# Kernel tuning notes

Hardware: AMD Instinct MI355X
Metric: run time of the kernel (lower is better)

The kernel has to match this reference:

```python
import jax, jax.numpy as jnp
import numpy as np

N_NODES = 40000
N_EDGES = 640000
D = 128
NEG_SLOPE = 0.2
EPS = 0.0  # init_eps=0, learn_eps=False -> constant buffer


def setup_inputs() -> dict:
    key = jax.random.key(0)
    ks = jax.random.split(key, 9)
    return {
        "feat": jax.random.normal(ks[0], (N_NODES, D), dtype=jnp.float32),
        "W_src": jax.random.normal(ks[1], (D, D), dtype=jnp.float32) * 0.1,
        "W_dst": jax.random.normal(ks[2], (D, D), dtype=jnp.float32) * 0.1,
        "W_src2": jax.random.normal(ks[3], (D, D), dtype=jnp.float32) * 0.1,
        "W_dst2": jax.random.normal(ks[4], (D, D), dtype=jnp.float32) * 0.1,
        "attn_l": jax.random.normal(ks[5], (D,), dtype=jnp.float32) * 0.1,
        "attn_r": jax.random.normal(ks[6], (D,), dtype=jnp.float32) * 0.1,
        "src": jax.random.randint(ks[7], (N_EDGES,), 0, N_NODES, dtype=jnp.int32),
        "dst": jax.random.randint(ks[8], (N_EDGES,), 0, N_NODES, dtype=jnp.int32),
    }


def reference(feat, W_src, W_dst, W_src2, W_dst2, attn_l, attn_r, src, dst):
    n = feat.shape[0]
    # Four linear projections (no bias), nn.Linear applies x @ W.T
    fs1 = feat @ W_src.T    # [N, D] -> messages for GIN sum
    fd1 = feat @ W_dst.T    # [N, D] -> self term
    fs2 = feat @ W_src2.T   # [N, D] -> attention-weighted messages
    fd2 = feat @ W_dst2.T   # [N, D]

    # GAT-style per-node attention logits
    el = jnp.sum(fs2 * attn_l, axis=-1)  # [N]
    er = jnp.sum(fd2 * attn_r, axis=-1)  # [N]

    # Per-edge score: u_add_v + leaky_relu
    e = el[src] + er[dst]                                   # [E]
    e = jnp.where(e >= 0, e, NEG_SLOPE * e)

    # edge_softmax: segment-wise softmax over edges grouped by dst
    seg_max = jax.ops.segment_max(e, dst, num_segments=n)   # [N]
    seg_max = jnp.where(jnp.isfinite(seg_max), seg_max, 0.0)
    ex = jnp.exp(e - seg_max[dst])                          # [E]
    denom = jax.ops.segment_sum(ex, dst, num_segments=n)    # [N]
    a = ex / denom[dst]                                     # [E]

    # update_all(copy_u, sum): plain neighbor sum of fs1
    neigh = jax.ops.segment_sum(fs1[src], dst, num_segments=n)            # [N, D]
    # update_all(u_mul_e, sum): attention-weighted sum of fs2
    add_ft = jax.ops.segment_sum(fs2[src] * a[:, None], dst, num_segments=n)  # [N, D]

    rst = (1.0 + EPS) * fd1 + neigh + add_ft
    return rst
```

## Files before the change

### kernel.cpp

```cpp
#include <hip/hip_runtime.h>
#include <math.h>

#define N_NODES 40000
#define N_EDGES 640000
#define D 128
#define NEG_SLOPE 0.2f
#define BCAP 64

typedef __bf16 bf16x8 __attribute__((ext_vector_type(8)));
typedef float f32x4 __attribute__((ext_vector_type(4)));

__device__ __forceinline__ unsigned short f2bf(float f) {
    unsigned int u = __float_as_uint(f);
    return (unsigned short)((u + 0x7fffu + ((u >> 16) & 1u)) >> 16);
}
__device__ __forceinline__ float bflo(unsigned int u) { return __uint_as_float(u << 16); }
__device__ __forceinline__ float bfhi(unsigned int u) { return __uint_as_float(u & 0xffff0000u); }

__global__ void k_zero_v(uint4* __restrict__ cnt4,
                         const float* __restrict__ Ws2, const float* __restrict__ Wd2,
                         const float* __restrict__ attn_l, const float* __restrict__ attn_r,
                         float* __restrict__ v_l, float* __restrict__ v_r) {
    if (blockIdx.x == 40) {
        int t = threadIdx.x;
        if (t < 128) {
            float s = 0.0f;
            for (int j = 0; j < D; ++j) s += attn_l[j] * Ws2[j * D + t];
            v_l[t] = s;
        } else {
            int k = t - 128;
            float s = 0.0f;
            for (int j = 0; j < D; ++j) s += attn_r[j] * Wd2[j * D + k];
            v_r[k] = s;
        }
        return;
    }
    int i = blockIdx.x * 256 + threadIdx.x;
    if (i < 10000) cnt4[i] = make_uint4(0, 0, 0, 0);
}

__global__ void k_setup(const float* __restrict__ Ws, const float* __restrict__ Ws2,
                        const float* __restrict__ Wd,
                        unsigned short* __restrict__ Wfrag,
                        const float* __restrict__ v_l, const float* __restrict__ v_r,
                        const int* __restrict__ src, const int* __restrict__ dst,
                        int* __restrict__ cnt, unsigned short* __restrict__ bucket,
                        const float* __restrict__ feat, unsigned int* __restrict__ featb,
                        float* __restrict__ el, float* __restrict__ er) {
    if (blockIdx.x >= 2692) {
        int idx = blockIdx.x - 2692;
        int row = idx * 16 + (threadIdx.x >> 4);
        int c   = threadIdx.x & 15;
        const float* fp = feat + (size_t)row * D + c * 8;
        float4 p = *(const float4*)fp;
        float4 q = *(const float4*)(fp + 4);
        uint4 u;
        u.x = (unsigned int)f2bf(p.x) | ((unsigned int)f2bf(p.y) << 16);
        u.y = (unsigned int)f2bf(p.z) | ((unsigned int)f2bf(p.w) << 16);
        u.z = (unsigned int)f2bf(q.x) | ((unsigned int)f2bf(q.y) << 16);
        u.w = (unsigned int)f2bf(q.z) | ((unsigned int)f2bf(q.w) << 16);
        *(uint4*)(featb + (size_t)row * 64 + c * 4) = u;
        const float* vlp = v_l + c * 8;
        const float* vrp = v_r + c * 8;
        float4 l0 = *(const float4*)vlp, l1 = *(const float4*)(vlp + 4);
        float4 r0 = *(const float4*)vrp, r1 = *(const float4*)(vrp + 4);
        float sl = p.x*l0.x + p.y*l0.y + p.z*l0.z + p.w*l0.w
                 + q.x*l1.x + q.y*l1.y + q.z*l1.z + q.w*l1.w;
        float sr = p.x*r0.x + p.y*r0.y + p.z*r0.z + p.w*r0.w
                 + q.x*r1.x + q.y*r1.y + q.z*r1.z + q.w*r1.w;
        #pragma unroll
        for (int w = 1; w <= 8; w <<= 1) {
            sl += __shfl_xor(sl, w);
            sr += __shfl_xor(sr, w);
        }
        if (c == 0) { el[row] = sl; er[row] = sr; }
        return;
    }
    if (blockIdx.x >= 192) {
        int e = (blockIdx.x - 192) * 256 + threadIdx.x;
        if (e < N_EDGES) {
            int d = dst[e];
            int slot = atomicAdd(&cnt[d], 1);
            if (slot < BCAP) bucket[(size_t)d * BCAP + slot] = (unsigned short)src[e];
        }
        return;
    }
    int idx = blockIdx.x * 256 + threadIdx.x;
    int e    = idx & 7;
    int lane = (idx >> 3) & 63;
    int ks   = (idx >> 9) & 3;
    int ct   = (idx >> 11) & 7;
    int m    = idx >> 14;
    int col  = ct * 16 + (lane & 15);
    int k    = ks * 32 + (lane >> 4) * 8 + e;
    const float* W = (m == 0) ? Ws : (m == 1) ? Ws2 : Wd;
    Wfrag[idx] = f2bf(W[col * D + k]);
}

__global__ __launch_bounds__(256) void k_aggregate(
    const int* __restrict__ cnt, const unsigned short* __restrict__ bucket,
    const float* __restrict__ el, const float* __restrict__ er,
    const unsigned int* __restrict__ featb,
    unsigned int* __restrict__ agg1b, unsigned int* __restrict__ agg2b)
{
    const int node = blockIdx.x * 4 + (threadIdx.x >> 6);
    const int lane = threadIdx.x & 63;
    if (node >= N_NODES) return;
    int deg = cnt[node];
    deg = (deg > BCAP) ? BCAP : deg;

    const int q = lane & 15;
    const int g = lane >> 4;
    float A1[8], A2[8];
    #pragma unroll
    for (int c = 0; c < 8; ++c) { A1[c] = 0.f; A2[c] = 0.f; }

    if (deg > 0) {
        const int base = node * BCAP;
        const float ern = er[node];
        int s_l = 0;
        float e = -INFINITY;
        if (lane < deg) {
            s_l = bucket[base + lane];
            e = el[s_l] + ern;
            e = (e >= 0.f) ? e : NEG_SLOPE * e;
        }
        float mx = e;
        #pragma unroll
        for (int w = 32; w >= 1; w >>= 1) mx = fmaxf(mx, __shfl_xor(mx, w));
        float p = (lane < deg) ? __expf(e - mx) : 0.f;
        float ssum = p;
        #pragma unroll
        for (int w = 32; w >= 1; w >>= 1) ssum += __shfl_xor(ssum, w);
        float a_l = p / ssum;

        const int dup = (deg + 15) & ~15;
        for (int i = 0; i < dup; i += 16) {
            uint4 v[4];
            float av[4], wf[4];
            #pragma unroll
            for (int j = 0; j < 4; ++j) {
                int eidx = i + j * 4 + g;
                int s = __shfl(s_l, eidx);
                av[j] = __shfl(a_l, eidx);
                wf[j] = (eidx < deg) ? 1.0f : 0.0f;
                v[j] = *(const uint4*)(featb + (size_t)s * 64 + q * 4);
            }
            #pragma unroll
            for (int j = 0; j < 4; ++j) {
                float x0 = bflo(v[j].x), x1 = bfhi(v[j].x);
                float x2 = bflo(v[j].y), x3 = bfhi(v[j].y);
                float x4 = bflo(v[j].z), x5 = bfhi(v[j].z);
                float x6 = bflo(v[j].w), x7 = bfhi(v[j].w);
                A1[0] += wf[j] * x0; A2[0] += av[j] * x0;
                A1[1] += wf[j] * x1; A2[1] += av[j] * x1;
                A1[2] += wf[j] * x2; A2[2] += av[j] * x2;
                A1[3] += wf[j] * x3; A2[3] += av[j] * x3;
                A1[4] += wf[j] * x4; A2[4] += av[j] * x4;
                A1[5] += wf[j] * x5; A2[5] += av[j] * x5;
                A1[6] += wf[j] * x6; A2[6] += av[j] * x6;
                A1[7] += wf[j] * x7; A2[7] += av[j] * x7;
            }
        }
        #pragma unroll
        for (int c = 0; c < 8; ++c) {
            A1[c] += __shfl_xor(A1[c], 16); A1[c] += __shfl_xor(A1[c], 32);
            A2[c] += __shfl_xor(A2[c], 16); A2[c] += __shfl_xor(A2[c], 32);
        }
    }

    if (lane < 16) {
        uint4 u1, u2;
        u1.x = (unsigned int)f2bf(A1[0]) | ((unsigned int)f2bf(A1[1]) << 16);
        u1.y = (unsigned int)f2bf(A1[2]) | ((unsigned int)f2bf(A1[3]) << 16);
        u1.z = (unsigned int)f2bf(A1[4]) | ((unsigned int)f2bf(A1[5]) << 16);
        u1.w = (unsigned int)f2bf(A1[6]) | ((unsigned int)f2bf(A1[7]) << 16);
        u2.x = (unsigned int)f2bf(A2[0]) | ((unsigned int)f2bf(A2[1]) << 16);
        u2.y = (unsigned int)f2bf(A2[2]) | ((unsigned int)f2bf(A2[3]) << 16);
        u2.z = (unsigned int)f2bf(A2[4]) | ((unsigned int)f2bf(A2[5]) << 16);
        u2.w = (unsigned int)f2bf(A2[6]) | ((unsigned int)f2bf(A2[7]) << 16);
        *(uint4*)(agg1b + (size_t)node * 64 + q * 4) = u1;
        *(uint4*)(agg2b + (size_t)node * 64 + q * 4) = u2;
    }
}

__global__ __launch_bounds__(256) void k_gemm_all(
    const unsigned int* __restrict__ featb,
    const unsigned int* __restrict__ agg1b, const unsigned int* __restrict__ agg2b,
    const unsigned short* __restrict__ Wfrag, float* __restrict__ out)
{
    const int lane = threadIdx.x & 63;
    const int wave = threadIdx.x >> 6;
    const int tile = blockIdx.x >> 1;
    const int cth  = (blockIdx.x & 1) * 4;
    const int row0 = tile * 64 + wave * 16;
    const int arow = row0 + (lane & 15);
    const int koff = (lane >> 4) * 4;

    bf16x8 af[4], a1[4], a2[4];
    #pragma unroll
    for (int ks = 0; ks < 4; ++ks) {
        size_t o = (size_t)arow * 64 + ks * 16 + koff;
        af[ks] = *(const bf16x8*)(featb + o);
        a1[ks] = *(const bf16x8*)(agg1b + o);
        a2[ks] = *(const bf16x8*)(agg2b + o);
    }

    const bf16x8* wf0 = (const bf16x8*)Wfrag;
    const bf16x8* wf1 = wf0 + (size_t)(8 * 4) * 64;
    const bf16x8* wf2 = wf0 + (size_t)(2 * 8 * 4) * 64;

    f32x4 acc[4];
    #pragma unroll
    for (int c = 0; c < 4; ++c) acc[c] = (f32x4){0.f, 0.f, 0.f, 0.f};
    #pragma unroll
    for (int ks = 0; ks < 4; ++ks) {
        #pragma unroll
        for (int c = 0; c < 4; ++c) {
            const size_t bo = (size_t)((cth + c) * 4 + ks) * 64 + lane;
            acc[c] = __builtin_amdgcn_mfma_f32_16x16x32_bf16(af[ks], wf2[bo], acc[c], 0, 0, 0);
            acc[c] = __builtin_amdgcn_mfma_f32_16x16x32_bf16(a1[ks], wf0[bo], acc[c], 0, 0, 0);
            acc[c] = __builtin_amdgcn_mfma_f32_16x16x32_bf16(a2[ks], wf1[bo], acc[c], 0, 0, 0);
        }
    }

    const int rbase = row0 + (lane >> 4) * 4;
    const int cbase = lane & 15;
    #pragma unroll
    for (int c = 0; c < 4; ++c)
        #pragma unroll
        for (int r = 0; r < 4; ++r)
            out[(size_t)(rbase + r) * D + (cth + c) * 16 + cbase] = acc[c][r];
}

extern "C" void kernel_launch(void* const* d_in, const int* in_sizes, int n_in,
                              void* d_out, int out_size, void* d_ws, size_t ws_size,
                              hipStream_t stream) {
    const float* feat   = (const float*)d_in[0];
    const float* W_src  = (const float*)d_in[1];
    const float* W_dst  = (const float*)d_in[2];
    const float* W_src2 = (const float*)d_in[3];
    const float* W_dst2 = (const float*)d_in[4];
    const float* attn_l = (const float*)d_in[5];
    const float* attn_r = (const float*)d_in[6];
    const int*   src    = (const int*)d_in[7];
    const int*   dst    = (const int*)d_in[8];
    float* out = (float*)d_out;

    char* w = (char*)d_ws;
    float* v_l = (float*)w;                       w += 128 * 4;
    float* v_r = (float*)w;                       w += 128 * 4;
    float* el  = (float*)w;                       w += N_NODES * 4;
    float* er  = (float*)w;                       w += N_NODES * 4;
    int* cnt   = (int*)w;                         w += N_NODES * 4;
    unsigned int* featb = (unsigned int*)w;       w += (size_t)N_NODES * 64 * 4;
    unsigned int* agg1b = (unsigned int*)w;       w += (size_t)N_NODES * 64 * 4;
    unsigned int* agg2b = (unsigned int*)w;       w += (size_t)N_NODES * 64 * 4;
    unsigned short* bucket = (unsigned short*)w;  w += (size_t)N_NODES * BCAP * 2;
    unsigned short* Wfrag = (unsigned short*)w;   w += 3 * 8 * 4 * 64 * 8 * 2;

    k_zero_v<<<41, 256, 0, stream>>>((uint4*)cnt, W_src2, W_dst2, attn_l, attn_r, v_l, v_r);

    k_setup<<<5192, 256, 0, stream>>>(W_src, W_src2, W_dst, Wfrag, v_l, v_r,
                                      src, dst, cnt, bucket, feat, featb, el, er);

    k_aggregate<<<(N_NODES + 3) / 4, 256, 0, stream>>>(cnt, bucket, el, er,
                                                       featb, agg1b, agg2b);

    k_gemm_all<<<1250, 256, 0, stream>>>(featb, agg1b, agg2b, Wfrag, out);
}
```

Before: 96.21 us.

## Prefetch first 32 neighbor rows before softmax and batch edge bucketing per thread

In the aggregate kernel, the first 32 neighbor feature rows are gathered before the softmax reduction runs, so gather latency overlaps the attention computation. The loop is split into an unconditional first 16, a conditional second 16, and a remainder loop. The setup kernel now processes four edges per thread in the bucketing blocks and reorders block roles so bucketing launches first, which reduces the grid size. This adds register pressure from eight uint4 prefetches and issues loads for padded lanes that all point at node 0.

```diff
diff --git a/kernel.cpp b/kernel.cpp
--- a/kernel.cpp
+++ b/kernel.cpp
@@ -47,54 +47,57 @@
                         int* __restrict__ cnt, unsigned short* __restrict__ bucket,
                         const float* __restrict__ feat, unsigned int* __restrict__ featb,
                         float* __restrict__ el, float* __restrict__ er) {
-    if (blockIdx.x >= 2692) {
-        int idx = blockIdx.x - 2692;
-        int row = idx * 16 + (threadIdx.x >> 4);
-        int c   = threadIdx.x & 15;
-        const float* fp = feat + (size_t)row * D + c * 8;
-        float4 p = *(const float4*)fp;
-        float4 q = *(const float4*)(fp + 4);
-        uint4 u;
-        u.x = (unsigned int)f2bf(p.x) | ((unsigned int)f2bf(p.y) << 16);
-        u.y = (unsigned int)f2bf(p.z) | ((unsigned int)f2bf(p.w) << 16);
-        u.z = (unsigned int)f2bf(q.x) | ((unsigned int)f2bf(q.y) << 16);
-        u.w = (unsigned int)f2bf(q.z) | ((unsigned int)f2bf(q.w) << 16);
-        *(uint4*)(featb + (size_t)row * 64 + c * 4) = u;
-        const float* vlp = v_l + c * 8;
-        const float* vrp = v_r + c * 8;
-        float4 l0 = *(const float4*)vlp, l1 = *(const float4*)(vlp + 4);
-        float4 r0 = *(const float4*)vrp, r1 = *(const float4*)(vrp + 4);
-        float sl = p.x*l0.x + p.y*l0.y + p.z*l0.z + p.w*l0.w
-                 + q.x*l1.x + q.y*l1.y + q.z*l1.z + q.w*l1.w;
-        float sr = p.x*r0.x + p.y*r0.y + p.z*r0.z + p.w*r0.w
-                 + q.x*r1.x + q.y*r1.y + q.z*r1.z + q.w*r1.w;
-        #pragma unroll
-        for (int w = 1; w <= 8; w <<= 1) {
-            sl += __shfl_xor(sl, w);
-            sr += __shfl_xor(sr, w);
-        }
-        if (c == 0) { el[row] = sl; er[row] = sr; }
+    if (blockIdx.x < 625) {
+        int t = blockIdx.x * 256 + threadIdx.x;
+        #pragma unroll
+        for (int j = 0; j < 4; ++j) {
+            int e = t + j * 160000;
+            int d = dst[e];
+            int s = src[e];
+            int slot = atomicAdd(&cnt[d], 1);
+            if (slot < BCAP) bucket[(size_t)d * BCAP + slot] = (unsigned short)s;
+        }
         return;
     }
-    if (blockIdx.x >= 192) {
-        int e = (blockIdx.x - 192) * 256 + threadIdx.x;
-        if (e < N_EDGES) {
-            int d = dst[e];
-            int slot = atomicAdd(&cnt[d], 1);
-            if (slot < BCAP) bucket[(size_t)d * BCAP + slot] = (unsigned short)src[e];
-        }
+    if (blockIdx.x < 817) {
+        int idx = (blockIdx.x - 625) * 256 + threadIdx.x;
+        int e    = idx & 7;
+        int lane = (idx >> 3) & 63;
+        int ks   = (idx >> 9) & 3;
+        int ct   = (idx >> 11) & 7;
+        int m    = idx >> 14;
+        int col  = ct * 16 + (lane & 15);
+        int k    = ks * 32 + (lane >> 4) * 8 + e;
+        const float* W = (m == 0) ? Ws : (m == 1) ? Ws2 : Wd;
+        Wfrag[idx] = f2bf(W[col * D + k]);
         return;
     }
-    int idx = blockIdx.x * 256 + threadIdx.x;
-    int e    = idx & 7;
-    int lane = (idx >> 3) & 63;
-    int ks   = (idx >> 9) & 3;
-    int ct   = (idx >> 11) & 7;
-    int m    = idx >> 14;
-    int col  = ct * 16 + (lane & 15);
-    int k    = ks * 32 + (lane >> 4) * 8 + e;
-    const float* W = (m == 0) ? Ws : (m == 1) ? Ws2 : Wd;
-    Wfrag[idx] = f2bf(W[col * D + k]);
+    int idx = blockIdx.x - 817;
+    int row = idx * 16 + (threadIdx.x >> 4);
+    int c   = threadIdx.x & 15;
+    const float* fp = feat + (size_t)row * D + c * 8;
+    float4 p = *(const float4*)fp;
+    float4 q = *(const float4*)(fp + 4);
+    uint4 u;
+    u.x = (unsigned int)f2bf(p.x) | ((unsigned int)f2bf(p.y) << 16);
+    u.y = (unsigned int)f2bf(p.z) | ((unsigned int)f2bf(p.w) << 16);
+    u.z = (unsigned int)f2bf(q.x) | ((unsigned int)f2bf(q.y) << 16);
+    u.w = (unsigned int)f2bf(q.z) | ((unsigned int)f2bf(q.w) << 16);
+    *(uint4*)(featb + (size_t)row * 64 + c * 4) = u;
+    const float* vlp = v_l + c * 8;
+    const float* vrp = v_r + c * 8;
+    float4 l0 = *(const float4*)vlp, l1 = *(const float4*)(vlp + 4);
+    float4 r0 = *(const float4*)vrp, r1 = *(const float4*)(vrp + 4);
+    float sl = p.x*l0.x + p.y*l0.y + p.z*l0.z + p.w*l0.w
+             + q.x*l1.x + q.y*l1.y + q.z*l1.z + q.w*l1.w;
+    float sr = p.x*r0.x + p.y*r0.y + p.z*r0.z + p.w*r0.w
+             + q.x*r1.x + q.y*r1.y + q.z*r1.z + q.w*r1.w;
+    #pragma unroll
+    for (int w = 1; w <= 8; w <<= 1) {
+        sl += __shfl_xor(sl, w);
+        sr += __shfl_xor(sr, w);
+    }
+    if (c == 0) { el[row] = sl; er[row] = sr; }
 }
 
 __global__ __launch_bounds__(256) void k_aggregate(
@@ -117,11 +120,20 @@
 
     if (deg > 0) {
         const int base = node * BCAP;
+        int s_l = bucket[base + lane];
+        if (lane >= deg) s_l = 0;
+
+        uint4 v[8];
+        #pragma unroll
+        for (int j = 0; j < 8; ++j) {
+            int eidx = (j >> 2) * 16 + (j & 3) * 4 + g;
+            int s = __shfl(s_l, eidx);
+            v[j] = *(const uint4*)(featb + (size_t)s * 64 + q * 4);
+        }
+
         const float ern = er[node];
-        int s_l = 0;
         float e = -INFINITY;
         if (lane < deg) {
-            s_l = bucket[base + lane];
             e = el[s_l] + ern;
             e = (e >= 0.f) ? e : NEG_SLOPE * e;
         }
@@ -134,34 +146,72 @@
         for (int w = 32; w >= 1; w >>= 1) ssum += __shfl_xor(ssum, w);
         float a_l = p / ssum;
 
-        const int dup = (deg + 15) & ~15;
-        for (int i = 0; i < dup; i += 16) {
-            uint4 v[4];
-            float av[4], wf[4];
+        #pragma unroll
+        for (int j = 0; j < 4; ++j) {
+            int eidx = (j & 3) * 4 + g;
+            float av = __shfl(a_l, eidx);
+            float wf = (eidx < deg) ? 1.0f : 0.0f;
+            float x0 = bflo(v[j].x), x1 = bfhi(v[j].x);
+            float x2 = bflo(v[j].y), x3 = bfhi(v[j].y);
+            float x4 = bflo(v[j].z), x5 = bfhi(v[j].z);
+            float x6 = bflo(v[j].w), x7 = bfhi(v[j].w);
+            A1[0] += wf * x0; A2[0] += av * x0;
+            A1[1] += wf * x1; A2[1] += av * x1;
+            A1[2] += wf * x2; A2[2] += av * x2;
+            A1[3] += wf * x3; A2[3] += av * x3;
+            A1[4] += wf * x4; A2[4] += av * x4;
+            A1[5] += wf * x5; A2[5] += av * x5;
+            A1[6] += wf * x6; A2[6] += av * x6;
+            A1[7] += wf * x7; A2[7] += av * x7;
+        }
+        if (deg > 16) {
             #pragma unroll
-            for (int j = 0; j < 4; ++j) {
-                int eidx = i + j * 4 + g;
-                int s = __shfl(s_l, eidx);
-                av[j] = __shfl(a_l, eidx);
-                wf[j] = (eidx < deg) ? 1.0f : 0.0f;
-                v[j] = *(const uint4*)(featb + (size_t)s * 64 + q * 4);
-            }
-            #pragma unroll
-            for (int j = 0; j < 4; ++j) {
+            for (int j = 4; j < 8; ++j) {
+                int eidx = 16 + (j & 3) * 4 + g;
+                float av = __shfl(a_l, eidx);
+                float wf = (eidx < deg) ? 1.0f : 0.0f;
                 float x0 = bflo(v[j].x), x1 = bfhi(v[j].x);
                 float x2 = bflo(v[j].y), x3 = bfhi(v[j].y);
                 float x4 = bflo(v[j].z), x5 = bfhi(v[j].z);
                 float x6 = bflo(v[j].w), x7 = bfhi(v[j].w);
-                A1[0] += wf[j] * x0; A2[0] += av[j] * x0;
-                A1[1] += wf[j] * x1; A2[1] += av[j] * x1;
-                A1[2] += wf[j] * x2; A2[2] += av[j] * x2;
-                A1[3] += wf[j] * x3; A2[3] += av[j] * x3;
-                A1[4] += wf[j] * x4; A2[4] += av[j] * x4;
-                A1[5] += wf[j] * x5; A2[5] += av[j] * x5;
-                A1[6] += wf[j] * x6; A2[6] += av[j] * x6;
-                A1[7] += wf[j] * x7; A2[7] += av[j] * x7;
+                A1[0] += wf * x0; A2[0] += av * x0;
+                A1[1] += wf * x1; A2[1] += av * x1;
+                A1[2] += wf * x2; A2[2] += av * x2;
+                A1[3] += wf * x3; A2[3] += av * x3;
+                A1[4] += wf * x4; A2[4] += av * x4;
+                A1[5] += wf * x5; A2[5] += av * x5;
+                A1[6] += wf * x6; A2[6] += av * x6;
+                A1[7] += wf * x7; A2[7] += av * x7;
             }
-        }
+            for (int i = 32; i < deg; i += 16) {
+                uint4 vt[4];
+                float av[4], wf[4];
+                #pragma unroll
+                for (int j = 0; j < 4; ++j) {
+                    int eidx = i + j * 4 + g;
+                    int s = __shfl(s_l, eidx);
+                    av[j] = __shfl(a_l, eidx);
+                    wf[j] = (eidx < deg) ? 1.0f : 0.0f;
+                    vt[j] = *(const uint4*)(featb + (size_t)s * 64 + q * 4);
+                }
+                #pragma unroll
+                for (int j = 0; j < 4; ++j) {
+                    float x0 = bflo(vt[j].x), x1 = bfhi(vt[j].x);
+                    float x2 = bflo(vt[j].y), x3 = bfhi(vt[j].y);
+                    float x4 = bflo(vt[j].z), x5 = bfhi(vt[j].z);
+                    float x6 = bflo(vt[j].w), x7 = bfhi(vt[j].w);
+                    A1[0] += wf[j] * x0; A2[0] += av[j] * x0;
+                    A1[1] += wf[j] * x1; A2[1] += av[j] * x1;
+                    A1[2] += wf[j] * x2; A2[2] += av[j] * x2;
+                    A1[3] += wf[j] * x3; A2[3] += av[j] * x3;
+                    A1[4] += wf[j] * x4; A2[4] += av[j] * x4;
+                    A1[5] += wf[j] * x5; A2[5] += av[j] * x5;
+                    A1[6] += wf[j] * x6; A2[6] += av[j] * x6;
+                    A1[7] += wf[j] * x7; A2[7] += av[j] * x7;
+                }
+            }
+        }
+
         #pragma unroll
         for (int c = 0; c < 8; ++c) {
             A1[c] += __shfl_xor(A1[c], 16); A1[c] += __shfl_xor(A1[c], 32);
@@ -261,7 +311,7 @@
 
     k_zero_v<<<41, 256, 0, stream>>>((uint4*)cnt, W_src2, W_dst2, attn_l, attn_r, v_l, v_r);
 
-    k_setup<<<5192, 256, 0, stream>>>(W_src, W_src2, W_dst, Wfrag, v_l, v_r,
+    k_setup<<<3317, 256, 0, stream>>>(W_src, W_src2, W_dst, Wfrag, v_l, v_r,
                                       src, dst, cnt, bucket, feat, featb, el, er);
 
     k_aggregate<<<(N_NODES + 3) / 4, 256, 0, stream>>>(cnt, bucket, el, er,
```

Result: slower. 98.73 us (+2.6%).

## Fuse neighbor aggregation and output GEMM into one kernel via LDS

Applied to the files above, without the earlier changes.

Merges the aggregation kernel and the MFMA GEMM kernel so each 1024-thread block aggregates 16 nodes into shared memory, then 8 waves compute the 16x128 output tile directly. This removes the global round-trip of the two bf16 aggregate buffers and one kernel launch. In exchange, half the waves sit idle during the GEMM phase, a block barrier is added, and each block reloads the weight fragments, with smaller GEMM tiles than before.

```diff
diff --git a/kernel.cpp b/kernel.cpp
--- a/kernel.cpp
+++ b/kernel.cpp
@@ -97,15 +97,19 @@
     Wfrag[idx] = f2bf(W[col * D + k]);
 }
 
-__global__ __launch_bounds__(256) void k_aggregate(
+__global__ __launch_bounds__(1024, 8) void k_agg_gemm(
     const int* __restrict__ cnt, const unsigned short* __restrict__ bucket,
     const float* __restrict__ el, const float* __restrict__ er,
-    const unsigned int* __restrict__ featb,
-    unsigned int* __restrict__ agg1b, unsigned int* __restrict__ agg2b)
+    const unsigned int* __restrict__ featb, const unsigned short* __restrict__ Wfrag,
+    float* __restrict__ out)
 {
-    const int node = blockIdx.x * 4 + (threadIdx.x >> 6);
+    __shared__ uint4 lds1[16][17];
+    __shared__ uint4 lds2[16][17];
+
+    const int wv   = threadIdx.x >> 6;
     const int lane = threadIdx.x & 63;
-    if (node >= N_NODES) return;
+    const int node = blockIdx.x * 16 + wv;
+
     int deg = cnt[node];
     deg = (deg > BCAP) ? BCAP : deg;
 
@@ -179,58 +183,38 @@
         u2.y = (unsigned int)f2bf(A2[2]) | ((unsigned int)f2bf(A2[3]) << 16);
         u2.z = (unsigned int)f2bf(A2[4]) | ((unsigned int)f2bf(A2[5]) << 16);
         u2.w = (unsigned int)f2bf(A2[6]) | ((unsigned int)f2bf(A2[7]) << 16);
-        *(uint4*)(agg1b + (size_t)node * 64 + q * 4) = u1;
-        *(uint4*)(agg2b + (size_t)node * 64 + q * 4) = u2;
-    }
-}
-
-__global__ __launch_bounds__(256) void k_gemm_all(
-    const unsigned int* __restrict__ featb,
-    const unsigned int* __restrict__ agg1b, const unsigned int* __restrict__ agg2b,
-    const unsigned short* __restrict__ Wfrag, float* __restrict__ out)
-{
-    const int lane = threadIdx.x & 63;
-    const int wave = threadIdx.x >> 6;
-    const int tile = blockIdx.x >> 1;
-    const int cth  = (blockIdx.x & 1) * 4;
-    const int row0 = tile * 64 + wave * 16;
-    const int arow = row0 + (lane & 15);
-    const int koff = (lane >> 4) * 4;
-
-    bf16x8 af[4], a1[4], a2[4];
-    #pragma unroll
-    for (int ks = 0; ks < 4; ++ks) {
-        size_t o = (size_t)arow * 64 + ks * 16 + koff;
-        af[ks] = *(const bf16x8*)(featb + o);
-        a1[ks] = *(const bf16x8*)(agg1b + o);
-        a2[ks] = *(const bf16x8*)(agg2b + o);
-    }
-
-    const bf16x8* wf0 = (const bf16x8*)Wfrag;
-    const bf16x8* wf1 = wf0 + (size_t)(8 * 4) * 64;
-    const bf16x8* wf2 = wf0 + (size_t)(2 * 8 * 4) * 64;
-
-    f32x4 acc[4];
-    #pragma unroll
-    for (int c = 0; c < 4; ++c) acc[c] = (f32x4){0.f, 0.f, 0.f, 0.f};
-    #pragma unroll
-    for (int ks = 0; ks < 4; ++ks) {
-        #pragma unroll
-        for (int c = 0; c < 4; ++c) {
-            const size_t bo = (size_t)((cth + c) * 4 + ks) * 64 + lane;
-            acc[c] = __builtin_amdgcn_mfma_f32_16x16x32_bf16(af[ks], wf2[bo], acc[c], 0, 0, 0);
-            acc[c] = __builtin_amdgcn_mfma_f32_16x16x32_bf16(a1[ks], wf0[bo], acc[c], 0, 0, 0);
-            acc[c] = __builtin_amdgcn_mfma_f32_16x16x32_bf16(a2[ks], wf1[bo], acc[c], 0, 0, 0);
-        }
-    }
-
-    const int rbase = row0 + (lane >> 4) * 4;
-    const int cbase = lane & 15;
-    #pragma unroll
-    for (int c = 0; c < 4; ++c)
-        #pragma unroll
-        for (int r = 0; r < 4; ++r)
-            out[(size_t)(rbase + r) * D + (cth + c) * 16 + cbase] = acc[c][r];
+        lds1[wv][q] = u1;
+        lds2[wv][q] = u2;
+    }
+    __syncthreads();
+
+    if (wv < 8) {
+        const int ct = wv;
+        const int r = lane & 15;
+        const int h = lane >> 4;
+        const int row0 = blockIdx.x * 16;
+
+        const bf16x8* wf0 = (const bf16x8*)Wfrag;
+        const bf16x8* wf1 = wf0 + (size_t)(8 * 4) * 64;
+        const bf16x8* wf2 = wf0 + (size_t)(2 * 8 * 4) * 64;
+
+        f32x4 acc = (f32x4){0.f, 0.f, 0.f, 0.f};
+        #pragma unroll
+        for (int ks = 0; ks < 4; ++ks) {
+            bf16x8 af = *(const bf16x8*)(featb + (size_t)(row0 + r) * 64 + ks * 16 + h * 4);
+            bf16x8 a1 = *(const bf16x8*)&lds1[r][ks * 4 + h];
+            bf16x8 a2 = *(const bf16x8*)&lds2[r][ks * 4 + h];
+            const size_t bo = (size_t)(ct * 4 + ks) * 64 + lane;
+            acc = __builtin_amdgcn_mfma_f32_16x16x32_bf16(af, wf2[bo], acc, 0, 0, 0);
+            acc = __builtin_amdgcn_mfma_f32_16x16x32_bf16(a1, wf0[bo], acc, 0, 0, 0);
+            acc = __builtin_amdgcn_mfma_f32_16x16x32_bf16(a2, wf1[bo], acc, 0, 0, 0);
+        }
+
+        const int rbase = row0 + h * 4;
+        #pragma unroll
+        for (int rr = 0; rr < 4; ++rr)
+            out[(size_t)(rbase + rr) * D + ct * 16 + r] = acc[rr];
+    }
 }
 
 extern "C" void kernel_launch(void* const* d_in, const int* in_sizes, int n_in,
@@ -254,8 +238,6 @@
     float* er  = (float*)w;                       w += N_NODES * 4;
     int* cnt   = (int*)w;                         w += N_NODES * 4;
     unsigned int* featb = (unsigned int*)w;       w += (size_t)N_NODES * 64 * 4;
-    unsigned int* agg1b = (unsigned int*)w;       w += (size_t)N_NODES * 64 * 4;
-    unsigned int* agg2b = (unsigned int*)w;       w += (size_t)N_NODES * 64 * 4;
     unsigned short* bucket = (unsigned short*)w;  w += (size_t)N_NODES * BCAP * 2;
     unsigned short* Wfrag = (unsigned short*)w;   w += 3 * 8 * 4 * 64 * 8 * 2;
 
@@ -264,8 +246,5 @@
     k_setup<<<5192, 256, 0, stream>>>(W_src, W_src2, W_dst, Wfrag, v_l, v_r,
                                       src, dst, cnt, bucket, feat, featb, el, er);
 
-    k_aggregate<<<(N_NODES + 3) / 4, 256, 0, stream>>>(cnt, bucket, el, er,
-                                                       featb, agg1b, agg2b);
-
-    k_gemm_all<<<1250, 256, 0, stream>>>(featb, agg1b, agg2b, Wfrag, out);
-}
+    k_agg_gemm<<<2500, 1024, 0, stream>>>(cnt, bucket, el, er, featb, Wfrag, out);
+}
```

Result: slower. 99.06 us (+3.0%).
